# Performance work log

Measured on AMD Instinct MI355X. Metric: run time of the kernel, lower is better.

The kernel has to match this reference:

```python
import jax, jax.numpy as jnp
import numpy as np

T, D_IN, D_OUT, L, R = 8192, 4096, 4096, 16, 16


def setup_inputs() -> dict:
    key = jax.random.key(0)
    ks = jax.random.split(key, 7)
    x = jax.random.normal(ks[0], (T, D_IN), dtype=jnp.float32)
    W = jax.random.normal(ks[1], (D_OUT, D_IN), dtype=jnp.float32) / np.sqrt(D_IN)
    base_bias = jax.random.normal(ks[2], (D_OUT,), dtype=jnp.float32)
    # stacked LoRA weights (squeezed over the dummy dim-1 in the torch code)
    lora_a = jax.random.normal(ks[3], (L, R, D_IN), dtype=jnp.float32) / np.sqrt(D_IN)
    lora_b = jax.random.normal(ks[4], (L, D_OUT, R), dtype=jnp.float32) / np.sqrt(R)
    bias_stacked = jax.random.normal(ks[5], (L, D_OUT), dtype=jnp.float32)
    # per-token adapter index in [-1, L); -1 means "no LoRA"
    indices = jax.random.randint(ks[6], (T,), -1, L, dtype=jnp.int32)
    return {"x": x, "W": W, "base_bias": base_bias, "lora_a": lora_a,
            "lora_b": lora_b, "bias_stacked": bias_stacked, "indices": indices}


def reference(x, W, base_bias, lora_a, lora_b, bias_stacked, indices):
    num_loras = lora_a.shape[0]
    # base dense GEMM + base bias (ReplicatedLinear.quant_method.apply)
    out = x @ W.T + base_bias  # [T, D_OUT]
    # one_hot gives an all-zero row for indices == -1, matching the masking
    # in apply_bias and the no-op semantics of add_lora for unmapped tokens.
    onehot = jax.nn.one_hot(indices, num_loras, dtype=x.dtype)  # [T, L]
    # per-adapter bias gather-scatter (apply_bias)
    out = out + onehot @ bias_stacked  # [T, D_OUT]
    # SGMV-style LoRA: shrink with A, expand with B, scatter-add into out.
    shrunk_all = jnp.einsum('td,lrd->ltr', x, lora_a)        # [L, T, R]
    shrunk = jnp.einsum('tl,ltr->tr', onehot, shrunk_all)    # [T, R] per-token
    masked = onehot[:, :, None] * shrunk[:, None, :]         # [T, L, R]
    out = out + jnp.einsum('tlr,lor->to', masked, lora_b)    # [T, D_OUT]
    return out
```

## Files before the change

kernel.cpp:

```cpp
#include <hip/hip_runtime.h>
#include <hip/hip_bf16.h>
#include <stdint.h>

typedef unsigned short u16;
typedef unsigned int u32;

#define T_TOK 8192
#define DIN   4096
#define DOUT  4096
#define NL    16
#define NR    16
#define KX    4096
#define K2    4416
#define NKT   69
#define GITERS 34

typedef __attribute__((ext_vector_type(8))) __bf16 bf16x8;
typedef __attribute__((ext_vector_type(4))) float  f32x4;

__device__ __forceinline__ u32 bf16rne(float f) {
    u32 x = __float_as_uint(f);
    return (x + 0x7FFFu + ((x >> 16) & 1u)) >> 16;
}
__device__ __forceinline__ u32 pack2(float a, float b) {
    return bf16rne(a) | (bf16rne(b) << 16);
}

__global__ void pack_mats(const float* __restrict__ x, const float* __restrict__ W,
                          u16* __restrict__ Abf, u16* __restrict__ Bbf) {
    const int total = (T_TOK + DOUT) * (DIN / 8);
    for (int i = blockIdx.x * blockDim.x + threadIdx.x; i < total;
         i += gridDim.x * blockDim.x) {
        int row = i >> 9;
        int c8  = (i & 511) << 3;
        const float* src;
        u16* dst;
        if (row < T_TOK) { src = x + (size_t)row * DIN; dst = Abf + (size_t)row * K2; }
        else { src = W + (size_t)(row - T_TOK) * DIN; dst = Bbf + (size_t)(row - T_TOK) * K2; }
        const float4* s = (const float4*)(src + c8);
        float4 f0 = s[0], f1 = s[1];
        uint4 u;
        u.x = pack2(f0.x, f0.y); u.y = pack2(f0.z, f0.w);
        u.z = pack2(f1.x, f1.y); u.w = pack2(f1.z, f1.w);
        *(uint4*)(dst + c8) = u;
    }
}

#define NBEX (DOUT * 320)
__global__ void pack_small(const float* __restrict__ lora_b,
                           const float* __restrict__ base_bias,
                           const float* __restrict__ bias_st,
                           const float* __restrict__ la,
                           u16* __restrict__ Bbf, u16* __restrict__ Aabf) {
    const int total = NBEX + NL * NR * DIN / 8;
    for (int i = blockIdx.x * blockDim.x + threadIdx.x; i < total;
         i += gridDim.x * blockDim.x) {
        if (i < NBEX) {
            int o = i / 320;
            int j = i - o * 320;
            float v = 0.f;
            if (j < 256) {
                int l = j >> 4, r = j & 15;
                v = lora_b[((size_t)l * DOUT + o) * NR + r];
            } else if (j == 256) {
                v = base_bias[o];
            } else if (j < 273) {
                v = bias_st[(size_t)(j - 257) * DOUT + o];
            }
            Bbf[(size_t)o * K2 + KX + j] = (u16)bf16rne(v);
        } else {
            int c8 = (i - NBEX) << 3;
            const float4* s = (const float4*)(la + c8);
            float4 f0 = s[0], f1 = s[1];
            uint4 u;
            u.x = pack2(f0.x, f0.y); u.y = pack2(f0.z, f0.w);
            u.z = pack2(f1.x, f1.y); u.w = pack2(f1.z, f1.w);
            *(uint4*)(Aabf + c8) = u;
        }
    }
}

__global__ __launch_bounds__(512) void zfill_kernel(const u16* __restrict__ Axr,
                                                    const u16* __restrict__ La,
                                                    const int* __restrict__ idx,
                                                    u16* __restrict__ Abf) {
    __shared__ u16 sX[2][64 * 64];
    __shared__ u16 sL[2][128 * 64];
    const int tid  = threadIdx.x;
    const int lane = tid & 63, wid = tid >> 6;
    const int wr = wid >> 2, wc = wid & 3;
    const int lrow = lane & 15;
    const int klo  = (lane >> 4) << 4;
    const int sxr  = (lrow & 7) << 4;
    const int kxb[2] = { klo ^ sxr, (64 + klo) ^ sxr };

    const int bt = blockIdx.x >> 1;
    const int nh = blockIdx.x & 1;

    const int r0 = tid >> 3;
    const int c4 = (tid & 7) ^ (r0 & 7);
    const u16* pX = Axr + (size_t)(bt * 64 + r0) * K2 + c4 * 8;
    const u16* pL = La + (size_t)(nh * 128 + r0) * DIN + c4 * 8;
    const u16* pL2 = La + (size_t)(nh * 128 + 64 + r0) * DIN + c4 * 8;

    f32x4 acc[2][2];
#pragma unroll
    for (int m = 0; m < 2; ++m)
#pragma unroll
        for (int n = 0; n < 2; ++n) { f32x4 z = {0.f,0.f,0.f,0.f}; acc[m][n] = z; }

#define STAGEZ(buf, kt)                                                                \
  do {                                                                                 \
    __builtin_amdgcn_global_load_lds(                                                  \
      (const __attribute__((address_space(1))) u32*)(pX + (size_t)(kt) * 64),          \
      (__attribute__((address_space(3))) u32*)(&sX[buf][tid * 8]), 16, 0, 0);          \
    __builtin_amdgcn_global_load_lds(                                                  \
      (const __attribute__((address_space(1))) u32*)(pL + (size_t)(kt) * 64),          \
      (__attribute__((address_space(3))) u32*)(&sL[buf][tid * 8]), 16, 0, 0);          \
    __builtin_amdgcn_global_load_lds(                                                  \
      (const __attribute__((address_space(1))) u32*)(pL2 + (size_t)(kt) * 64),         \
      (__attribute__((address_space(3))) u32*)(&sL[buf][4096 + tid * 8]), 16, 0, 0);   \
  } while (0)

    STAGEZ(0, 0);
    for (int kt = 0; kt < 64; ++kt) {
        const int cur = kt & 1;
        if (kt < 63) {
            STAGEZ(cur ^ 1, kt + 1);
            asm volatile("s_waitcnt vmcnt(3)" ::: "memory");
        } else {
            asm volatile("s_waitcnt vmcnt(0)" ::: "memory");
        }
        __builtin_amdgcn_sched_barrier(0);
        __builtin_amdgcn_s_barrier();
        __builtin_amdgcn_sched_barrier(0);
        const char* sx = (const char*)sX[cur];
        const char* sl = (const char*)sL[cur];
        bf16x8 a[2][2], b[2][2];
#pragma unroll
        for (int m = 0; m < 2; ++m)
#pragma unroll
            for (int kk = 0; kk < 2; ++kk)
                a[m][kk] = *(const bf16x8*)(sx + (wr * 32 + m * 16 + lrow) * 128 + kxb[kk]);
#pragma unroll
        for (int n = 0; n < 2; ++n)
#pragma unroll
            for (int kk = 0; kk < 2; ++kk)
                b[n][kk] = *(const bf16x8*)(sl + (wc * 32 + n * 16 + lrow) * 128 + kxb[kk]);
#pragma unroll
        for (int m = 0; m < 2; ++m)
#pragma unroll
            for (int n = 0; n < 2; ++n)
#pragma unroll
                for (int kk = 0; kk < 2; ++kk)
                    acc[m][n] = __builtin_amdgcn_mfma_f32_16x16x32_bf16(
                        a[m][kk], b[n][kk], acc[m][n], 0, 0, 0);
        __builtin_amdgcn_sched_barrier(0);
        __builtin_amdgcn_s_barrier();
        __builtin_amdgcn_sched_barrier(0);
    }

#pragma unroll
    for (int m = 0; m < 2; ++m) {
#pragma unroll
        for (int rg = 0; rg < 4; ++rg) {
            int tl = wr * 32 + m * 16 + ((lane >> 4) << 2) + rg;
            int t  = bt * 64 + tl;
            int l  = idx[t];
#pragma unroll
            for (int n = 0; n < 2; ++n) {
                int col = nh * 128 + wc * 32 + n * 16 + (lane & 15);
                u16 v = ((col >> 4) == l) ? (u16)bf16rne(acc[m][n][rg]) : (u16)0;
                Abf[(size_t)t * K2 + KX + col] = v;
            }
        }
    }
    if (nh == 0) {
        int tl = tid >> 3, c8 = (tid & 7) * 8;
        int t = bt * 64 + tl;
        int l = idx[t];
        u32 w[4];
#pragma unroll
        for (int q = 0; q < 4; ++q) {
            int c0 = KX + 256 + c8 + 2 * q;
            u32 v0 = (c0 == 4352 || (l >= 0 && c0 == 4353 + l)) ? 0x3F80u : 0u;
            int c1 = c0 + 1;
            u32 v1 = (c1 == 4352 || (l >= 0 && c1 == 4353 + l)) ? 0x3F80u : 0u;
            w[q] = v0 | (v1 << 16);
        }
        *(uint4*)(Abf + (size_t)t * K2 + KX + 256 + c8) = *(uint4*)w;
    }
}


#define SBAR() __builtin_amdgcn_sched_barrier(0)
#define HWBAR() __builtin_amdgcn_s_barrier()
#define PHASE_BAR() do { SBAR(); HWBAR(); SBAR(); } while (0)
#define VMCNT4() asm volatile("s_waitcnt vmcnt(4)" ::: "memory")
#define VMCNT0() asm volatile("s_waitcnt vmcnt(0)" ::: "memory")

#define STAGE(ptr, h, buf, seg, kt)                                                   \
  do { if ((kt) < NKT) {                                                              \
    __builtin_amdgcn_global_load_lds(                                                 \
      (const __attribute__((address_space(1))) u32*)((ptr) + (size_t)((h)*128 + 0)*K2 + (size_t)(kt)*64),  \
      (__attribute__((address_space(3))) u32*)(lds16 + ((((buf)*4+(seg))<<13) + tid*8)), 16, 0, 0);        \
    __builtin_amdgcn_global_load_lds(                                                 \
      (const __attribute__((address_space(1))) u32*)((ptr) + (size_t)((h)*128 + 64)*K2 + (size_t)(kt)*64), \
      (__attribute__((address_space(3))) u32*)(lds16 + ((((buf)*4+(seg))<<13) + tid*8 + 4096)), 16, 0, 0); \
  } } while (0)

#define RD_AH(buf, mh, aa)                                                            \
  { _Pragma("unroll") for (int mm = 0; mm < 4; ++mm)                                  \
    _Pragma("unroll") for (int kk = 0; kk < 2; ++kk)                                  \
      aa[mm][kk] = *(const bf16x8*)(smem + (((buf)*4 + wr) << 14) + lrow*128          \
          + (mh)*8192 + mm*2048 + kxb[kk]); }

#define RD_BH(buf, nh, bf)                                                            \
  { _Pragma("unroll") for (int nn = 0; nn < 2; ++nn)                                  \
    _Pragma("unroll") for (int kk = 0; kk < 2; ++kk)                                  \
      bf[nn][kk] = *(const bf16x8*)(smem + (((buf)*4 + 2 + (wc>>1)) << 14)            \
          + ((wc&1)*64 + lrow)*128 + ((nh)*2+nn)*2048 + kxb[kk]); }

#define MMQ(mh, nh, aa, bf)                                                           \
  { __builtin_amdgcn_s_setprio(1);                                                    \
    _Pragma("unroll") for (int mm = 0; mm < 4; ++mm)                                  \
    _Pragma("unroll") for (int nn = 0; nn < 2; ++nn)                                  \
    _Pragma("unroll") for (int kk = 0; kk < 2; ++kk)                                  \
      acc[(mh)*4+mm][(nh)*2+nn] = __builtin_amdgcn_mfma_f32_16x16x32_bf16(            \
          aa[mm][kk], bf[nn][kk], acc[(mh)*4+mm][(nh)*2+nn], 0, 0, 0);                \
    __builtin_amdgcn_s_setprio(0); }

__global__ __launch_bounds__(512, 2) void gemm_kernel(const u16* __restrict__ A,
                                                      const u16* __restrict__ B,
                                                      float* __restrict__ C) {
    __shared__ u16 lds16[65536];
    const char* smem = (const char*)lds16;

    const int tid  = threadIdx.x;
    const int lane = tid & 63, wid = tid >> 6;
    const int wr = wid >> 2, wc = wid & 3;
    const int lrow = lane & 15;
    const int klo  = (lane >> 4) << 4;
    const int sx   = (lrow & 7) << 4;
    const int kxb[2] = { klo ^ sx, (64 + klo) ^ sx };

    const int wg  = blockIdx.x;
    const int swz = (wg & 7) * 64 + (wg >> 3);
    const int bm = swz >> 4;
    const int bn = swz & 15;

    const int r0  = tid >> 3;
    const int sc4 = (tid & 7) ^ (r0 & 7);
    const u16* pA = A + (size_t)(bm * 256 + r0) * K2 + sc4 * 8;
    const u16* pB = B + (size_t)(bn * 256 + r0) * K2 + sc4 * 8;

    f32x4 acc[8][4];
#pragma unroll
    for (int m = 0; m < 8; ++m)
#pragma unroll
        for (int n = 0; n < 4; ++n) { f32x4 z = {0.f,0.f,0.f,0.f}; acc[m][n] = z; }
    bf16x8 a0[4][2], a1[4][2], bA[2][2], bB[2][2];

    STAGE(pA, 0, 0, 0, 0); STAGE(pA, 1, 0, 1, 0);
    STAGE(pB, 0, 0, 2, 0); STAGE(pB, 1, 0, 3, 0);
    STAGE(pA, 0, 1, 0, 1); STAGE(pA, 1, 1, 1, 1);
    VMCNT4();
    PHASE_BAR();

    for (int i = 0; i < GITERS; ++i) {
        const int k1 = 2 * i + 1, kn = 2 * i + 2, kn1 = 2 * i + 3;
        RD_AH(0, 0, a0); RD_BH(0, 0, bA);
        STAGE(pB, 0, 1, 2, k1);
        MMQ(0, 0, a0, bA);
        PHASE_BAR();
        RD_AH(0, 1, a1);
        STAGE(pB, 1, 1, 3, k1);
        MMQ(1, 0, a1, bA);
        PHASE_BAR();
        RD_BH(0, 1, bB);
        STAGE(pA, 0, 0, 0, kn);
        MMQ(0, 1, a0, bB);
        PHASE_BAR();
        STAGE(pA, 1, 0, 1, kn);
        MMQ(1, 1, a1, bB);
        VMCNT4();
        PHASE_BAR();
        RD_AH(1, 0, a0); RD_BH(1, 0, bA);
        STAGE(pB, 0, 0, 2, kn);
        MMQ(0, 0, a0, bA);
        PHASE_BAR();
        RD_AH(1, 1, a1);
        STAGE(pB, 1, 0, 3, kn);
        MMQ(1, 0, a1, bA);
        PHASE_BAR();
        RD_BH(1, 1, bB);
        STAGE(pA, 0, 1, 0, kn1);
        MMQ(0, 1, a0, bB);
        PHASE_BAR();
        STAGE(pA, 1, 1, 1, kn1);
        MMQ(1, 1, a1, bB);
        VMCNT4();
        PHASE_BAR();
    }

    VMCNT0();
    PHASE_BAR();
    RD_AH(0, 0, a0); RD_AH(0, 1, a1); RD_BH(0, 0, bA); RD_BH(0, 1, bB);
    MMQ(0, 0, a0, bA); MMQ(1, 0, a1, bA); MMQ(0, 1, a0, bB); MMQ(1, 1, a1, bB);

    const int crow0 = bm * 256 + wr * 128 + ((lane >> 4) << 2);
    const int ccol0 = bn * 256 + wc * 64 + (lane & 15);
#pragma unroll
    for (int m = 0; m < 8; ++m)
#pragma unroll
        for (int n = 0; n < 4; ++n)
#pragma unroll
            for (int rg = 0; rg < 4; ++rg)
                C[(size_t)(crow0 + m * 16 + rg) * DOUT + ccol0 + n * 16] = acc[m][n][rg];
}


extern "C" void kernel_launch(void* const* d_in, const int* in_sizes, int n_in,
                              void* d_out, int out_size, void* d_ws, size_t ws_size,
                              hipStream_t stream) {
    const float* x         = (const float*)d_in[0];
    const float* W         = (const float*)d_in[1];
    const float* base_bias = (const float*)d_in[2];
    const float* lora_a    = (const float*)d_in[3];
    const float* lora_b    = (const float*)d_in[4];
    const float* bias_st   = (const float*)d_in[5];
    const int*   indices   = (const int*)d_in[6];
    float* out = (float*)d_out;

    u16* Abf  = (u16*)d_ws;
    u16* Bbf  = Abf + (size_t)T_TOK * K2;
    u16* Aabf = Bbf + (size_t)DOUT * K2;

    pack_mats<<<6144, 256, 0, stream>>>(x, W, Abf, Bbf);
    pack_small<<<1536, 256, 0, stream>>>(lora_b, base_bias, bias_st, lora_a, Bbf, Aabf);
    zfill_kernel<<<256, 512, 0, stream>>>(Abf, Aabf, indices, Abf);
    gemm_kernel<<<512, 512, 0, stream>>>(Abf, Bbf, out);
    (void)in_sizes; (void)n_in; (void)out_size; (void)ws_size;
}
```

Measured before the change: 341.5 us.

## Restructure GEMM main loop into four phases with paired A/B staging

Regroups the pipelined bf16 GEMM main loop from eight barrier-separated phases per double iteration into four. Each phase now reads more LDS fragments and issues two MFMA quadrants, and the global-to-LDS stage order and prefetch slots are reshuffled to match. The aim is to halve the number of workgroup barriers and give more compute per phase to cover the loads. In exchange, LDS buffer reuse timing changes, more registers are live per phase, and any ordering mistake could race on the shared buffers.

Result: no change. 346.5 us (+1.5%).

```diff
diff --git a/kernel.cpp b/kernel.cpp
--- a/kernel.cpp
+++ b/kernel.cpp
@@ -263,42 +263,28 @@
 
     STAGE(pA, 0, 0, 0, 0); STAGE(pA, 1, 0, 1, 0);
     STAGE(pB, 0, 0, 2, 0); STAGE(pB, 1, 0, 3, 0);
-    STAGE(pA, 0, 1, 0, 1); STAGE(pA, 1, 1, 1, 1);
+    STAGE(pA, 0, 1, 0, 1); STAGE(pB, 0, 1, 2, 1);
     VMCNT4();
     PHASE_BAR();
 
     for (int i = 0; i < GITERS; ++i) {
-        const int k1 = 2 * i + 1, kn = 2 * i + 2, kn1 = 2 * i + 3;
-        RD_AH(0, 0, a0); RD_BH(0, 0, bA);
-        STAGE(pB, 0, 1, 2, k1);
-        MMQ(0, 0, a0, bA);
+        const int kO = 2 * i + 1, kE2 = 2 * i + 2, kO2 = 2 * i + 3;
+        RD_AH(0, 0, a0); RD_BH(0, 0, bA); RD_BH(0, 1, bB);
+        STAGE(pA, 1, 1, 1, kO); STAGE(pB, 1, 1, 3, kO);
+        MMQ(0, 0, a0, bA); MMQ(0, 1, a0, bB);
         PHASE_BAR();
         RD_AH(0, 1, a1);
-        STAGE(pB, 1, 1, 3, k1);
-        MMQ(1, 0, a1, bA);
-        PHASE_BAR();
-        RD_BH(0, 1, bB);
-        STAGE(pA, 0, 0, 0, kn);
-        MMQ(0, 1, a0, bB);
-        PHASE_BAR();
-        STAGE(pA, 1, 0, 1, kn);
-        MMQ(1, 1, a1, bB);
+        STAGE(pA, 0, 0, 0, kE2); STAGE(pB, 0, 0, 2, kE2);
+        MMQ(1, 0, a1, bA); MMQ(1, 1, a1, bB);
         VMCNT4();
         PHASE_BAR();
-        RD_AH(1, 0, a0); RD_BH(1, 0, bA);
-        STAGE(pB, 0, 0, 2, kn);
-        MMQ(0, 0, a0, bA);
+        RD_AH(1, 0, a0); RD_BH(1, 0, bA); RD_BH(1, 1, bB);
+        STAGE(pA, 1, 0, 1, kE2); STAGE(pB, 1, 0, 3, kE2);
+        MMQ(0, 0, a0, bA); MMQ(0, 1, a0, bB);
         PHASE_BAR();
         RD_AH(1, 1, a1);
-        STAGE(pB, 1, 0, 3, kn);
-        MMQ(1, 0, a1, bA);
-        PHASE_BAR();
-        RD_BH(1, 1, bB);
-        STAGE(pA, 0, 1, 0, kn1);
-        MMQ(0, 1, a0, bB);
-        PHASE_BAR();
-        STAGE(pA, 1, 1, 1, kn1);
-        MMQ(1, 1, a1, bB);
+        STAGE(pA, 0, 1, 0, kO2); STAGE(pB, 0, 1, 2, kO2);
+        MMQ(1, 0, a1, bA); MMQ(1, 1, a1, bB);
         VMCNT4();
         PHASE_BAR();
     }
```
